# Kernel tuning notes

Hardware: AMD Instinct MI355X
Metric: run time of the kernel (lower is better)

Reference implementation:

```python
import jax, jax.numpy as jnp
import numpy as np

EPS = 1e-4

@jax.custom_vjp
def binarize(x):
    # BinaryConnectDeterministic: sign with sign(0)=+1
    return jnp.where(x >= 0, 1.0, -1.0).astype(x.dtype)

def _bin_fwd(x):
    return binarize(x), x

def _bin_bwd(x, g):
    # straight-through estimator, clipped to |x| <= 1
    return (g * (jnp.abs(x) <= 1).astype(g.dtype),)

binarize.defvjp(_bin_fwd, _bin_bwd)

def ap2(x):
    # approximate power-of-2: sign(x) * 2^round(log2|x|); grad is 0 a.e. (round/sign)
    a = jnp.maximum(jnp.abs(x), 1e-38)
    return jnp.sign(x) * jnp.exp2(jnp.round(jnp.log2(a)))

def shift_bn(x, gamma, beta, axes):
    # shift-based batch norm (BNN paper): var approximated via centered*AP2(centered),
    # inverse std and gamma replaced by their AP2 approximations. Training-mode batch stats.
    mean = jnp.mean(x, axis=axes, keepdims=True)
    c = x - mean
    var = jnp.mean(c * ap2(c), axis=axes, keepdims=True)
    xhat = c * ap2(1.0 / jnp.sqrt(var + EPS))
    shape = [1] * x.ndim
    shape[1] = x.shape[1]
    return ap2(gamma.reshape(shape)) * xhat + beta.reshape(shape)

def conv_bin(x, w, b):
    y = jax.lax.conv_general_dilated(x, binarize(w), (1, 1), [(1, 1), (1, 1)],
                                     dimension_numbers=('NCHW', 'OIHW', 'NCHW'))
    return y + b[None, :, None, None]

def maxpool3s2(x):
    return jax.lax.reduce_window(x, -jnp.inf, jax.lax.max,
                                 (1, 1, 3, 3), (1, 1, 2, 2), 'VALID')


def setup_inputs() -> dict:
    key = jax.random.key(0)
    ks = jax.random.split(key, 8)
    B, NU = 2048, 2048
    inp = {
        'x': jax.random.normal(ks[0], (B, 784), jnp.float32),
        'conv1_w': jax.random.normal(ks[1], (32, 1, 3, 3), jnp.float32) * 0.1,
        'conv1_b': jnp.zeros((32,), jnp.float32),
        'g1': jnp.ones((32,), jnp.float32), 'b1': jnp.zeros((32,), jnp.float32),
        'conv2_w': jax.random.normal(ks[2], (64, 32, 3, 3), jnp.float32) * 0.1,
        'conv2_b': jnp.zeros((64,), jnp.float32),
        'g2': jnp.ones((64,), jnp.float32), 'b2': jnp.zeros((64,), jnp.float32),
        'lin3_w': jax.random.normal(ks[3], (NU, 10816), jnp.float32) * 0.02,
        'lin3_b': jnp.zeros((NU,), jnp.float32),
        'g3': jnp.ones((NU,), jnp.float32), 'b3': jnp.zeros((NU,), jnp.float32),
        'lin4_w': jax.random.normal(ks[4], (10, NU), jnp.float32) * 0.02,
        'lin4_b': jnp.zeros((10,), jnp.float32),
    }
    return inp


def reference(x, conv1_w, conv1_b, g1, b1, conv2_w, conv2_b, g2, b2,
              lin3_w, lin3_b, g3, b3, lin4_w, lin4_b):
    h = x.reshape(-1, 1, 28, 28)
    h = jax.nn.relu(conv_bin(h, conv1_w, conv1_b))
    h = shift_bn(h, g1, b1, axes=(0, 2, 3))
    h = binarize(h)
    h = jax.nn.relu(conv_bin(h, conv2_w, conv2_b))
    h = maxpool3s2(h)                       # [B,64,13,13]
    h = shift_bn(h, g2, b2, axes=(0, 2, 3))
    h = binarize(h)
    h = h.reshape(h.shape[0], -1)           # [B,10816]
    h = jax.nn.relu(h @ binarize(lin3_w).T + lin3_b)
    h = shift_bn(h, g3, b3, axes=(0,))
    h = binarize(h)
    return h @ binarize(lin4_w).T + lin4_b  # [B,10] (no norm4/logsoftmax in forward)
```

## Files before the change

### kernel.cpp

```cpp
#include <hip/hip_runtime.h>

#define BB 2048
#define IMG 784
#define HWD 28
#define C1 32
#define C2 64
#define PP 169
#define PD 13
#define F3 10816
#define N3 2048
#define K4W 32
#define NOUT 10
#define CONV 27
#define PADW 30
#define OCCHUNK 8
#define IMGC 29
#define SCRP 740

typedef unsigned long long u64;
typedef int v4i __attribute__((ext_vector_type(4)));
typedef int v16i __attribute__((ext_vector_type(16)));

__device__ __forceinline__ float ap2mag(float c) {
    unsigned int a = __float_as_uint(c) & 0x7fffffffu;
    unsigned int e = (a >> 23) + ((a & 0x7fffffu) > 0x3504f3u);
    return __uint_as_float(e << 23);
}
__device__ __forceinline__ float ap2sgn(float g) {
    unsigned int u = __float_as_uint(g);
    unsigned int a = u & 0x7fffffffu;
    if (a == 0) return 0.f;
    unsigned int e = (a >> 23) + ((a & 0x7fffffu) > 0x3504f3u);
    return __uint_as_float((u & 0x80000000u) | (e << 23));
}

__global__ __launch_bounds__(256) void stage0(const float* __restrict__ x,
                                              const float* __restrict__ w1, const float* __restrict__ cb1,
                                              float* __restrict__ part1, float* __restrict__ w1b,
                                              const float* __restrict__ w2, char* __restrict__ w2i8,
                                              const float* __restrict__ w3, char* __restrict__ wp3i,
                                              const float* __restrict__ w4, u64* __restrict__ wp4) {
    __shared__ float xs[30 * PADW];
    __shared__ float red[4 * C1];
    int n = blockIdx.x, tid = threadIdx.x;
    int lane = tid & 63, wv = tid >> 6;
    {
        int idx = n * 256 + tid;
        int nthr = gridDim.x * 256;
        int total = (N3 * F3) / 4;
        for (int t = idx; t < total; t += nthr) {
            float4 wv4 = *(const float4*)(w3 + (size_t)t * 4);
            unsigned int w = (wv4.x >= 0.f ? 0x01u : 0xffu)
                           | (wv4.y >= 0.f ? 0x01u : 0xffu) << 8
                           | (wv4.z >= 0.f ? 0x01u : 0xffu) << 16
                           | (wv4.w >= 0.f ? 0x01u : 0xffu) << 24;
            *(unsigned int*)(wp3i + (size_t)t * 4) = w;
        }
    }
    if (n == 0) {
        for (int i = tid; i < C1 * 9; i += 256) w1b[i] = (w1[i] >= 0.f) ? 1.f : -1.f;
    } else if (n == 1) {
        for (int i = tid; i < 2 * 9 * 64 * 16; i += 256) {
            int hf = i / 9216;
            int r = i - hf * 9216;
            int t = r >> 10;
            int l = (r >> 4) & 63;
            int j = i & 15;
            int oc = hf * 32 + (l & 31);
            int ic = ((l >> 5) << 4) + j;
            w2i8[i] = (w2[oc * 288 + ic * 9 + t] >= 0.f) ? (char)1 : (char)(-1);
        }
    } else if (n == 2) {
        for (int w = wv; w < NOUT * K4W; w += 4) {
            int o = w / K4W, j = w % K4W;
            float wvl = w4[o * N3 + j * 64 + lane];
            u64 mask = __ballot(wvl >= 0.f);
            if (lane == 0) wp4[w] = mask;
        }
    }
    for (int i = tid; i < 30 * PADW; i += 256) {
        int r = i / PADW - 1, c = i % PADW - 1;
        float v = 0.f;
        if (r >= 0 && r < HWD && c >= 0 && c < HWD) v = x[n * IMG + r * HWD + c];
        xs[i] = v;
    }
    __syncthreads();
    bool act = tid < 196;
    int r = tid / 7, c0 = (tid % 7) * 4;
    float win[18];
#pragma unroll
    for (int k = 0; k < 18; k++) win[k] = 0.f;
    if (act) {
#pragma unroll
        for (int ry = 0; ry < 3; ry++)
#pragma unroll
            for (int cx = 0; cx < 6; cx++)
                win[ry * 6 + cx] = xs[(r + ry) * PADW + c0 + cx];
    }
#pragma unroll
    for (int ch = 0; ch < C1; ch++) {
        float a = 0.f;
        if (act) {
            float k0 = (w1[ch * 9 + 0] >= 0.f) ? 1.f : -1.f, k1 = (w1[ch * 9 + 1] >= 0.f) ? 1.f : -1.f;
            float k2 = (w1[ch * 9 + 2] >= 0.f) ? 1.f : -1.f, k3 = (w1[ch * 9 + 3] >= 0.f) ? 1.f : -1.f;
            float k4 = (w1[ch * 9 + 4] >= 0.f) ? 1.f : -1.f, k5 = (w1[ch * 9 + 5] >= 0.f) ? 1.f : -1.f;
            float k6 = (w1[ch * 9 + 6] >= 0.f) ? 1.f : -1.f, k7 = (w1[ch * 9 + 7] >= 0.f) ? 1.f : -1.f;
            float k8 = (w1[ch * 9 + 8] >= 0.f) ? 1.f : -1.f;
            float b = cb1[ch];
#pragma unroll
            for (int px = 0; px < 4; px++) {
                float s = win[px] * k0 + win[px + 1] * k1 + win[px + 2] * k2
                        + win[6 + px] * k3 + win[7 + px] * k4 + win[8 + px] * k5
                        + win[12 + px] * k6 + win[13 + px] * k7 + win[14 + px] * k8;
                a += fmaxf(s + b, 0.f);
            }
        }
        for (int off = 32; off; off >>= 1) a += __shfl_down(a, off);
        if (lane == 0) red[wv * C1 + ch] = a;
    }
    __syncthreads();
    if (tid < C1) part1[n * C1 + tid] = red[tid] + red[C1 + tid] + red[2 * C1 + tid] + red[3 * C1 + tid];
}

__global__ __launch_bounds__(256) void conv1_var(const float* __restrict__ x,
                            const float* __restrict__ w1b,
                            const float* __restrict__ cb1, const float* __restrict__ mean1,
                            float* __restrict__ part) {
    __shared__ float xs[30 * PADW];
    __shared__ float red[4 * C1];
    int n = blockIdx.x, tid = threadIdx.x;
    for (int i = tid; i < 30 * PADW; i += 256) {
        int r = i / PADW - 1, c = i % PADW - 1;
        float v = 0.f;
        if (r >= 0 && r < HWD && c >= 0 && c < HWD) v = x[n * IMG + r * HWD + c];
        xs[i] = v;
    }
    __syncthreads();
    bool act = tid < 196;
    int r = tid / 7, c0 = (tid % 7) * 4;
    float win[18];
#pragma unroll
    for (int k = 0; k < 18; k++) win[k] = 0.f;
    if (act) {
#pragma unroll
        for (int ry = 0; ry < 3; ry++)
#pragma unroll
            for (int cx = 0; cx < 6; cx++)
                win[ry * 6 + cx] = xs[(r + ry) * PADW + c0 + cx];
    }
    int lane = tid & 63, wv = tid >> 6;
#pragma unroll
    for (int ch = 0; ch < C1; ch++) {
        float a = 0.f;
        if (act) {
            float k0 = w1b[ch * 9 + 0], k1 = w1b[ch * 9 + 1], k2 = w1b[ch * 9 + 2];
            float k3 = w1b[ch * 9 + 3], k4 = w1b[ch * 9 + 4], k5 = w1b[ch * 9 + 5];
            float k6 = w1b[ch * 9 + 6], k7 = w1b[ch * 9 + 7], k8 = w1b[ch * 9 + 8];
            float b = cb1[ch], m = mean1[ch];
#pragma unroll
            for (int px = 0; px < 4; px++) {
                float s = win[px] * k0 + win[px + 1] * k1 + win[px + 2] * k2
                        + win[6 + px] * k3 + win[7 + px] * k4 + win[8 + px] * k5
                        + win[12 + px] * k6 + win[13 + px] * k7 + win[14 + px] * k8;
                float v = fmaxf(s + b, 0.f);
                float c = v - m;
                a += fabsf(c) * ap2mag(c);
            }
        }
        for (int off = 32; off; off >>= 1) a += __shfl_down(a, off);
        if (lane == 0) red[wv * C1 + ch] = a;
    }
    __syncthreads();
    if (tid < C1) part[n * C1 + tid] = red[tid] + red[C1 + tid] + red[2 * C1 + tid] + red[3 * C1 + tid];
}

__global__ __launch_bounds__(256) void conv1_pack(const float* __restrict__ x,
                           const float* __restrict__ w1b,
                           const float* __restrict__ cb1, const float* __restrict__ mean1,
                           const float* __restrict__ scale1, const float* __restrict__ beta1,
                           unsigned int* __restrict__ s1p) {
    __shared__ float xs[30 * PADW];
    int n = blockIdx.x, tid = threadIdx.x;
    for (int i = tid; i < 30 * PADW; i += 256) {
        int r = i / PADW - 1, c = i % PADW - 1;
        float v = 0.f;
        if (r >= 0 && r < HWD && c >= 0 && c < HWD) v = x[n * IMG + r * HWD + c];
        xs[i] = v;
    }
    __syncthreads();
    if (tid >= 196) return;
    int r = tid / 7, c0 = (tid % 7) * 4;
    float win[18];
#pragma unroll
    for (int ry = 0; ry < 3; ry++)
#pragma unroll
        for (int cx = 0; cx < 6; cx++)
            win[ry * 6 + cx] = xs[(r + ry) * PADW + c0 + cx];
    unsigned int bits0 = 0, bits1 = 0, bits2 = 0, bits3 = 0;
#pragma unroll
    for (int ch = 0; ch < C1; ch++) {
        float k0 = w1b[ch * 9 + 0], k1 = w1b[ch * 9 + 1], k2 = w1b[ch * 9 + 2];
        float k3 = w1b[ch * 9 + 3], k4 = w1b[ch * 9 + 4], k5 = w1b[ch * 9 + 5];
        float k6 = w1b[ch * 9 + 6], k7 = w1b[ch * 9 + 7], k8 = w1b[ch * 9 + 8];
        float b = cb1[ch], m = mean1[ch], sc = scale1[ch], bt = beta1[ch];
#pragma unroll
        for (int px = 0; px < 4; px++) {
            float s = win[px] * k0 + win[px + 1] * k1 + win[px + 2] * k2
                    + win[6 + px] * k3 + win[7 + px] * k4 + win[8 + px] * k5
                    + win[12 + px] * k6 + win[13 + px] * k7 + win[14 + px] * k8;
            float v = fmaxf(s + b, 0.f);
            float val = sc * (v - m) + bt;
            unsigned int bit = (val >= 0.f ? 1u : 0u) << ch;
            if (px == 0) bits0 |= bit;
            else if (px == 1) bits1 |= bit;
            else if (px == 2) bits2 |= bit;
            else bits3 |= bit;
        }
    }
    uint4 w4v = make_uint4(bits0, bits1, bits2, bits3);
    *reinterpret_cast<uint4*>(&s1p[n * IMG + r * HWD + c0]) = w4v;
}

__global__ __launch_bounds__(256) void conv2pool(const unsigned int* __restrict__ s1p,
                                                 const char* __restrict__ w2i8,
                                                 const float* __restrict__ cb2,
                                                 short* __restrict__ p2i,
                                                 float* __restrict__ part2) {
    __shared__ char img[IMGC * IMGC * 32];
    __shared__ short scr[32 * SCRP];
    __shared__ float psum[OCCHUNK * PP];
    __shared__ float pm[C2];
    int n = blockIdx.x, tid = threadIdx.x;
    int lane = tid & 63, wv = tid >> 6;
    for (int i = tid; i < IMGC * IMGC; i += 256) {
        int r = i / IMGC, c = i - r * IMGC;
        unsigned int w = 0u;
        if (r >= 1 && c >= 1) w = s1p[n * IMG + (r - 1) * HWD + (c - 1)];
        unsigned int d[8];
        if (r == 0 || c == 0) {
#pragma unroll
            for (int e = 0; e < 8; e++) d[e] = 0u;
        } else {
#pragma unroll
            for (int e = 0; e < 8; e++) {
                unsigned int nib = (w >> (4 * e)) & 0xFu;
                unsigned int t = (nib & 1u) | ((nib & 2u) << 7) | ((nib & 4u) << 14) | ((nib & 8u) << 21);
                d[e] = 0xFFFFFFFFu - t * 0xFEu;
            }
        }
        *(uint4*)&img[i * 32] = make_uint4(d[0], d[1], d[2], d[3]);
        *(uint4*)&img[i * 32 + 16] = make_uint4(d[4], d[5], d[6], d[7]);
    }
    __syncthreads();
    int hh = lane >> 5;
    int l31 = lane & 31;
    for (int hf = 0; hf < 2; hf++) {
        v4i bf[9];
#pragma unroll
        for (int t = 0; t < 9; t++)
            bf[t] = *(const v4i*)(w2i8 + (hf * 9 + t) * 1024 + lane * 16);
#pragma unroll
        for (int j = 0; j < 3; j++) {
            int mtA = wv + 8 * j, mtB = mtA + 4;
            int pA = mtA * 32 + l31; if (pA > 728) pA = 728;
            int pB = mtB * 32 + l31; if (pB > 728) pB = 728;
            int yA = pA / 27, xA = pA - yA * 27;
            int yB = pB / 27, xB = pB - yB * 27;
            int aA = (yA * IMGC + xA) * 32 + hh * 16;
            int aB = (yB * IMGC + xB) * 32 + hh * 16;
            v16i accA = {0,0,0,0,0,0,0,0,0,0,0,0,0,0,0,0};
            v16i accB = {0,0,0,0,0,0,0,0,0,0,0,0,0,0,0,0};
#pragma unroll
            for (int ky = 0; ky < 3; ky++)
#pragma unroll
                for (int kx = 0; kx < 3; kx++) {
                    v4i fA = *(const v4i*)&img[aA + (ky * IMGC + kx) * 32];
                    v4i fB = *(const v4i*)&img[aB + (ky * IMGC + kx) * 32];
                    accA = __builtin_amdgcn_mfma_i32_32x32x32_i8(fA, bf[ky * 3 + kx], accA, 0, 0, 0);
                    accB = __builtin_amdgcn_mfma_i32_32x32x32_i8(fB, bf[ky * 3 + kx], accB, 0, 0, 0);
                }
            short* sr = &scr[l31 * SCRP];
#pragma unroll
            for (int g = 0; g < 4; g++) {
                short4 sA;
                sA.x = (short)accA[4 * g + 0]; sA.y = (short)accA[4 * g + 1];
                sA.z = (short)accA[4 * g + 2]; sA.w = (short)accA[4 * g + 3];
                *(short4*)&sr[mtA * 32 + g * 8 + 4 * hh] = sA;
            }
            if (mtB < 23) {
#pragma unroll
                for (int g = 0; g < 4; g++) {
                    short4 sB;
                    sB.x = (short)accB[4 * g + 0]; sB.y = (short)accB[4 * g + 1];
                    sB.z = (short)accB[4 * g + 2]; sB.w = (short)accB[4 * g + 3];
                    *(short4*)&sr[mtB * 32 + g * 8 + 4 * hh] = sB;
                }
            }
        }
        __syncthreads();
        for (int base = 0; base < 32; base += OCCHUNK) {
            for (int q = tid; q < OCCHUNK * PP; q += 256) {
                int ol = q / PP, pix = q - ol * PP;
                int py = pix / PD, px = pix - py * PD;
                const short* rr = &scr[(base + ol) * SCRP + (2 * py) * CONV + 2 * px];
                int m0 = max(max((int)rr[0], (int)rr[1]), (int)rr[2]);
                int m1 = max(max((int)rr[CONV], (int)rr[CONV + 1]), (int)rr[CONV + 2]);
                int m2 = max(max((int)rr[2 * CONV], (int)rr[2 * CONV + 1]), (int)rr[2 * CONV + 2]);
                int val = max(max(m0, m1), m2);
                int oc = hf * 32 + base + ol;
                p2i[n * F3 + oc * PP + pix] = (short)val;
                psum[q] = fmaxf((float)val + cb2[oc], 0.f);
            }
            __syncthreads();
            for (int ol = wv; ol < OCCHUNK; ol += 4) {
                float a = 0.f;
                for (int pp = lane; pp < PP; pp += 64) a += psum[ol * PP + pp];
                for (int off = 32; off; off >>= 1) a += __shfl_down(a, off);
                if (lane == 0) pm[hf * 32 + base + ol] = a;
            }
            __syncthreads();
        }
    }
    if (tid < C2) part2[n * C2 + tid] = pm[tid];
}

__global__ __launch_bounds__(256) void p2_var(const short* __restrict__ p2i,
                         const float* __restrict__ cb2,
                         const float* __restrict__ mean2, float* __restrict__ part) {
    int n = blockIdx.x, tid = threadIdx.x, lane = tid & 63, wv = tid >> 6;
    const short* rowb = p2i + (size_t)n * F3;
    __shared__ float red[C2];
#pragma unroll
    for (int i = 0; i < 16; i++) {
        int ch = wv * 16 + i;
        const short* row = rowb + ch * PP;
        float b = cb2[ch];
        float m = mean2[ch];
        float a = 0.f;
        for (int p = lane; p < PP; p += 64) {
            float v = fmaxf((float)row[p] + b, 0.f);
            float c = v - m;
            a += fabsf(c) * ap2mag(c);
        }
        for (int off = 32; off; off >>= 1) a += __shfl_down(a, off);
        if (lane == 0) red[ch] = a;
    }
    __syncthreads();
    if (tid < C2) part[n * C2 + tid] = red[tid];
}

__global__ __launch_bounds__(256) void reduce_stats(const float* __restrict__ part, int nch, int nblk,
                             const float* __restrict__ g, float* __restrict__ outv,
                             int mode, double count) {
    int ch = blockIdx.x, tid = threadIdx.x;
    double a = 0.0;
    for (int i = tid; i < nblk; i += 256) a += (double)part[(size_t)i * nch + ch];
    __shared__ double red[4];
    for (int off = 32; off; off >>= 1) a += __shfl_down(a, off);
    int lane = tid & 63, wv = tid >> 6;
    if (lane == 0) red[wv] = a;
    __syncthreads();
    if (tid == 0) {
        double s = red[0] + red[1] + red[2] + red[3];
        if (mode == 0) {
            outv[ch] = (float)(s / count);
        } else {
            float var = (float)(s / count);
            float inv = 1.0f / sqrtf(var + 1e-4f);
            outv[ch] = ap2sgn(g[ch]) * ap2mag(inv);
        }
    }
}

__global__ __launch_bounds__(256) void p2_packi8(const short* __restrict__ p2i, const float* __restrict__ cb2,
                        const float* __restrict__ mean2, const float* __restrict__ scale2,
                        const float* __restrict__ beta2, char* __restrict__ hp3i) {
    int idx = blockIdx.x * 256 + threadIdx.x;
    int nthr = gridDim.x * 256;
    int total = (BB * F3) / 4;
    for (int t = idx; t < total; t += nthr) {
        int base = t * 4;
        int f0 = base % F3;
        unsigned int w = 0;
#pragma unroll
        for (int e = 0; e < 4; e++) {
            int f = f0 + e;
            int oc = f / PP;
            float v = fmaxf((float)p2i[base + e] + cb2[oc], 0.f);
            float val = scale2[oc] * (v - mean2[oc]) + beta2[oc];
            w |= (val >= 0.f ? 0x01u : 0xffu) << (8 * e);
        }
        *(unsigned int*)(hp3i + base) = w;
    }
}

__global__ __launch_bounds__(256) void lin3_mfma(const char* __restrict__ hp3i,
                                                 const char* __restrict__ wp3i,
                                                 const float* __restrict__ b3l,
                                                 float* __restrict__ h3,
                                                 float* __restrict__ part3) {
    __shared__ v4i aL[2][512];
    __shared__ v4i bL[2][256];
    __shared__ float csr[4][32];
    int tid = threadIdx.x;
    int lane = tid & 63, wv = tid >> 6;
    int wr = wv >> 1, wc = wv & 1;
    int m0 = blockIdx.y * 128, n0 = blockIdx.x * 64;
    int ra = tid >> 1, ha = tid & 1;
    const char* ag = hp3i + (size_t)(m0 + ra) * F3 + ha * 32;
    int abase = (ra >> 4) * 64 + (2 * ha) * 16 + (ra & 15);
    int rb = tid >> 2, qb = tid & 3;
    const char* bg = wp3i + (size_t)(n0 + rb) * F3 + qb * 16;
    int bbase = (rb >> 4) * 64 + qb * 16 + (rb & 15);
    v4i acc[4][2];
#pragma unroll
    for (int i = 0; i < 4; i++)
#pragma unroll
        for (int j = 0; j < 2; j++) acc[i][j] = (v4i){0, 0, 0, 0};
    v4i a0 = *(const v4i*)ag, a1 = *(const v4i*)(ag + 16);
    v4i b0 = *(const v4i*)bg;
    aL[0][abase] = a0; aL[0][abase + 16] = a1;
    bL[0][bbase] = b0;
    __syncthreads();
    for (int c = 0; c < 169; c++) {
        int cur = c & 1, nxt = cur ^ 1;
        if (c < 168) {
            ag += 64; bg += 64;
            a0 = *(const v4i*)ag; a1 = *(const v4i*)(ag + 16);
            b0 = *(const v4i*)bg;
        }
        v4i af[4], bf[2];
#pragma unroll
        for (int i = 0; i < 4; i++) af[i] = aL[cur][(wr * 4 + i) * 64 + lane];
#pragma unroll
        for (int j = 0; j < 2; j++) bf[j] = bL[cur][(wc * 2 + j) * 64 + lane];
#pragma unroll
        for (int i = 0; i < 4; i++)
#pragma unroll
            for (int j = 0; j < 2; j++)
                acc[i][j] = __builtin_amdgcn_mfma_i32_16x16x64_i8(af[i], bf[j], acc[i][j], 0, 0, 0);
        if (c < 168) {
            aL[nxt][abase] = a0; aL[nxt][abase + 16] = a1;
            bL[nxt][bbase] = b0;
        }
        __syncthreads();
    }
    int q = lane >> 4, m16 = lane & 15;
    float cs[2] = {0.f, 0.f};
#pragma unroll
    for (int j = 0; j < 2; j++) {
        int col = n0 + wc * 32 + j * 16 + m16;
        float bias = b3l[col];
#pragma unroll
        for (int i = 0; i < 4; i++) {
            int rowb = m0 + wr * 64 + i * 16 + q * 4;
#pragma unroll
            for (int rg = 0; rg < 4; rg++) {
                float v = fmaxf((float)acc[i][j][rg] + bias, 0.f);
                h3[(size_t)(rowb + rg) * N3 + col] = v;
                cs[j] += v;
            }
        }
    }
#pragma unroll
    for (int j = 0; j < 2; j++) {
        cs[j] += __shfl_xor(cs[j], 16);
        cs[j] += __shfl_xor(cs[j], 32);
        if (lane < 16) csr[wv][j * 16 + m16] = cs[j];
    }
    __syncthreads();
    if (tid < 64) {
        int wcc = tid >> 5, cc = tid & 31;
        part3[(size_t)blockIdx.y * N3 + n0 + tid] = csr[wcc][cc] + csr[2 + wcc][cc];
    }
}

__global__ __launch_bounds__(256) void h3_finish(const float* __restrict__ h3,
                                                 const float* __restrict__ part3,
                                                 const float* __restrict__ g3,
                                                 float* __restrict__ mean3, float* __restrict__ scale3) {
    int nn = blockIdx.x, tid = threadIdx.x;
    __shared__ float msh;
    __shared__ double redd[4];
    if (tid < 64) {
        float a = (tid < 16) ? part3[(size_t)tid * N3 + nn] : 0.f;
        for (int off = 8; off; off >>= 1) a += __shfl_down(a, off);
        if (tid == 0) { float m = a / (float)BB; mean3[nn] = m; msh = m; }
    }
    __syncthreads();
    float m = msh;
    float acc = 0.f;
#pragma unroll
    for (int q = 0; q < 8; q++) {
        float v = h3[(size_t)(q * 256 + tid) * N3 + nn];
        float c = v - m;
        acc += fabsf(c) * ap2mag(c);
    }
    double a = (double)acc;
    for (int off = 32; off; off >>= 1) a += __shfl_down(a, off);
    int lane = tid & 63, wv = tid >> 6;
    if (lane == 0) redd[wv] = a;
    __syncthreads();
    if (tid == 0) {
        float var = (float)((redd[0] + redd[1] + redd[2] + redd[3]) / (double)BB);
        float inv = 1.0f / sqrtf(var + 1e-4f);
        scale3[nn] = ap2sgn(g3[nn]) * ap2mag(inv);
    }
}

__global__ __launch_bounds__(256) void h4_out(const float* __restrict__ h3,
                                              const float* __restrict__ mean3, const float* __restrict__ scale3,
                                              const float* __restrict__ bt3,
                                              const u64* __restrict__ wp4, const float* __restrict__ b4,
                                              float* __restrict__ out) {
    __shared__ u64 hb[K4W];
    __shared__ u64 wsh[NOUT * 33];
    int m = blockIdx.x, tid = threadIdx.x, lane = tid & 63, wv = tid >> 6;
    for (int i = tid; i < NOUT * K4W; i += 256) wsh[(i / K4W) * 33 + (i % K4W)] = wp4[i];
#pragma unroll
    for (int q = 0; q < 8; q++) {
        int j = wv * 8 + q;
        int f = j * 64 + lane;
        float v = h3[(size_t)m * N3 + f];
        float val = scale3[f] * (v - mean3[f]) + bt3[f];
        u64 mask = __ballot(val >= 0.f);
        if (lane == 0) hb[j] = mask;
    }
    __syncthreads();
    if (tid < NOUT) {
        int c = 0;
#pragma unroll
        for (int k = 0; k < K4W; k++) c += (int)__popcll(hb[k] ^ wsh[tid * 33 + k]);
        out[m * NOUT + tid] = (float)(N3 - 2 * c) + b4[tid];
    }
}

extern "C" void kernel_launch(void* const* d_in, const int* in_sizes, int n_in,
                              void* d_out, int out_size, void* d_ws, size_t ws_size,
                              hipStream_t stream) {
    const float* x   = (const float*)d_in[0];
    const float* w1  = (const float*)d_in[1];
    const float* cb1 = (const float*)d_in[2];
    const float* g1  = (const float*)d_in[3];
    const float* bt1 = (const float*)d_in[4];
    const float* w2  = (const float*)d_in[5];
    const float* cb2 = (const float*)d_in[6];
    const float* g2  = (const float*)d_in[7];
    const float* bt2 = (const float*)d_in[8];
    const float* w3  = (const float*)d_in[9];
    const float* b3l = (const float*)d_in[10];
    const float* g3  = (const float*)d_in[11];
    const float* bt3 = (const float*)d_in[12];
    const float* w4  = (const float*)d_in[13];
    const float* b4l = (const float*)d_in[14];
    float* out = (float*)d_out;

    char* base = (char*)d_ws;
    size_t off = 0;
    auto carve = [&](size_t bytes) { char* p = base + off; off = (off + bytes + 255) & ~(size_t)255; return p; };
    char* bufA = carve((size_t)BB * C2 * PP * 2);
    char* bufB = carve((size_t)BB * F3);
    char* bufC = carve((size_t)N3 * F3);
    short* p2i         = (short*)bufA;
    float* h3          = (float*)bufA;
    char* hp3i         = bufB;
    unsigned int* s1p  = (unsigned int*)bufB;
    char* wp3i         = bufC;
    u64* wp4           = (u64*)carve((size_t)NOUT * K4W * 8);
    char* w2i8         = (char*)carve((size_t)2 * 9 * 64 * 16);
    float* w1b         = (float*)carve((size_t)C1 * 9 * 4);
    float* part1       = (float*)carve((size_t)BB * C1 * 4);
    float* part2       = (float*)carve((size_t)BB * C2 * 4);
    float* part3       = (float*)carve((size_t)16 * N3 * 4);
    float* fstats      = (float*)carve((size_t)(32 + 32 + 64 + 64 + 2048 + 2048) * 4);
    float* mean1 = fstats;          float* scale1 = fstats + 32;
    float* mean2 = fstats + 64;     float* scale2 = fstats + 128;
    float* mean3 = fstats + 192;    float* scale3 = fstats + 2240;

    stage0<<<BB, 256, 0, stream>>>(x, w1, cb1, part1, w1b, w2, w2i8, w3, wp3i, w4, wp4);
    reduce_stats<<<C1, 256, 0, stream>>>(part1, C1, BB, g1, mean1, 0, (double)BB * IMG);
    conv1_var<<<BB, 256, 0, stream>>>(x, w1b, cb1, mean1, part1);
    reduce_stats<<<C1, 256, 0, stream>>>(part1, C1, BB, g1, scale1, 1, (double)BB * IMG);
    conv1_pack<<<BB, 256, 0, stream>>>(x, w1b, cb1, mean1, scale1, bt1, s1p);
    conv2pool<<<BB, 256, 0, stream>>>(s1p, w2i8, cb2, p2i, part2);
    reduce_stats<<<C2, 256, 0, stream>>>(part2, C2, BB, g2, mean2, 0, (double)BB * PP);
    p2_var<<<BB, 256, 0, stream>>>(p2i, cb2, mean2, part2);
    reduce_stats<<<C2, 256, 0, stream>>>(part2, C2, BB, g2, scale2, 1, (double)BB * PP);
    p2_packi8<<<2048, 256, 0, stream>>>(p2i, cb2, mean2, scale2, bt2, hp3i);
    lin3_mfma<<<dim3(32, 16), 256, 0, stream>>>(hp3i, wp3i, b3l, h3, part3);
    h3_finish<<<N3, 256, 0, stream>>>(h3, part3, g3, mean3, scale3);
    h4_out<<<BB, 256, 0, stream>>>(h3, mean3, scale3, bt3, wp4, b4l, out);

    (void)in_sizes; (void)n_in; (void)out_size; (void)ws_size;
}
```

Measured before the change: 580.0 us.

## Use direct global-to-LDS loads in lin3 GEMM and write transposed h3 for stats

The int8 GEMM main loop now loads operand tiles with global_load_lds straight into shared memory, double-buffered over 128-byte K chunks, so tiles no longer pass through registers before the LDS store. This halves the number of barrier iterations and doubles the LDS footprint. The epilogue also writes a column-major copy of h3, so h3_finish can read each column contiguously instead of with a large stride. The cost is an extra 16 MB store and larger shared-memory use per block, which may reduce occupancy.

Result: faster. 549.9 us (-5.2%).

```diff
diff --git a/kernel.cpp b/kernel.cpp
--- a/kernel.cpp
+++ b/kernel.cpp
@@ -20,6 +20,10 @@
 typedef unsigned long long u64;
 typedef int v4i __attribute__((ext_vector_type(4)));
 typedef int v16i __attribute__((ext_vector_type(16)));
+
+#define GLOAD16(gp, lp) __builtin_amdgcn_global_load_lds( \
+    (__attribute__((address_space(1))) void*)(gp),        \
+    (__attribute__((address_space(3))) void*)(lp), 16, 0, 0)
 
 __device__ __forceinline__ float ap2mag(float c) {
     unsigned int a = __float_as_uint(c) & 0x7fffffffu;
@@ -398,50 +402,66 @@
                                                  const char* __restrict__ wp3i,
                                                  const float* __restrict__ b3l,
                                                  float* __restrict__ h3,
+                                                 float* __restrict__ h3T,
                                                  float* __restrict__ part3) {
-    __shared__ v4i aL[2][512];
-    __shared__ v4i bL[2][256];
+    __shared__ v4i aL[2][1024];
+    __shared__ v4i bL[2][512];
     __shared__ float csr[4][32];
     int tid = threadIdx.x;
     int lane = tid & 63, wv = tid >> 6;
     int wr = wv >> 1, wc = wv & 1;
     int m0 = blockIdx.y * 128, n0 = blockIdx.x * 64;
-    int ra = tid >> 1, ha = tid & 1;
-    const char* ag = hp3i + (size_t)(m0 + ra) * F3 + ha * 32;
-    int abase = (ra >> 4) * 64 + (2 * ha) * 16 + (ra & 15);
-    int rb = tid >> 2, qb = tid & 3;
-    const char* bg = wp3i + (size_t)(n0 + rb) * F3 + qb * 16;
-    int bbase = (rb >> 4) * 64 + qb * 16 + (rb & 15);
+    int loff = (lane & 15) * F3 + (lane >> 4) * 16;
+    const char* gA0 = hp3i + (size_t)(m0 + wv * 16) * F3 + loff;
+    const char* gA1 = gA0 + (size_t)64 * F3;
+    const char* gB0 = wp3i + (size_t)(n0 + wv * 16) * F3 + loff;
+    char* ldsA = (char*)&aL[0][0];
+    char* ldsB = (char*)&bL[0][0];
+    int sA = wv * 1024, sB = wv * 1024;
     v4i acc[4][2];
 #pragma unroll
     for (int i = 0; i < 4; i++)
 #pragma unroll
         for (int j = 0; j < 2; j++) acc[i][j] = (v4i){0, 0, 0, 0};
-    v4i a0 = *(const v4i*)ag, a1 = *(const v4i*)(ag + 16);
-    v4i b0 = *(const v4i*)bg;
-    aL[0][abase] = a0; aL[0][abase + 16] = a1;
-    bL[0][bbase] = b0;
-    __syncthreads();
-    for (int c = 0; c < 169; c++) {
-        int cur = c & 1, nxt = cur ^ 1;
-        if (c < 168) {
-            ag += 64; bg += 64;
-            a0 = *(const v4i*)ag; a1 = *(const v4i*)(ag + 16);
-            b0 = *(const v4i*)bg;
-        }
-        v4i af[4], bf[2];
-#pragma unroll
-        for (int i = 0; i < 4; i++) af[i] = aL[cur][(wr * 4 + i) * 64 + lane];
-#pragma unroll
-        for (int j = 0; j < 2; j++) bf[j] = bL[cur][(wc * 2 + j) * 64 + lane];
-#pragma unroll
-        for (int i = 0; i < 4; i++)
-#pragma unroll
-            for (int j = 0; j < 2; j++)
-                acc[i][j] = __builtin_amdgcn_mfma_i32_16x16x64_i8(af[i], bf[j], acc[i][j], 0, 0, 0);
-        if (c < 168) {
-            aL[nxt][abase] = a0; aL[nxt][abase + 16] = a1;
-            bL[nxt][bbase] = b0;
+    GLOAD16(gA0,      ldsA + sA);
+    GLOAD16(gA1,      ldsA + sA + 4096);
+    GLOAD16(gA0 + 64, ldsA + sA + 8192);
+    GLOAD16(gA1 + 64, ldsA + sA + 12288);
+    GLOAD16(gB0,      ldsB + sB);
+    GLOAD16(gB0 + 64, ldsB + sB + 4096);
+    __syncthreads();
+    for (int c = 0; c <= 84; ++c) {
+        int cur = c & 1;
+        if (c < 84) {
+            int nb = cur ^ 1;
+            const char* pA0 = gA0 + (size_t)(c + 1) * 128;
+            const char* pA1 = gA1 + (size_t)(c + 1) * 128;
+            const char* pB0 = gB0 + (size_t)(c + 1) * 128;
+            char* dA = ldsA + nb * 16384 + sA;
+            char* dB = ldsB + nb * 8192 + sB;
+            GLOAD16(pA0, dA);
+            GLOAD16(pA1, dA + 4096);
+            GLOAD16(pB0, dB);
+            if (c + 1 < 84) {
+                GLOAD16(pA0 + 64, dA + 8192);
+                GLOAD16(pA1 + 64, dA + 12288);
+                GLOAD16(pB0 + 64, dB + 4096);
+            }
+        }
+        const v4i* aC = &aL[cur][0];
+        const v4i* bC = &bL[cur][0];
+        int nks = (c == 84) ? 1 : 2;
+        for (int ks = 0; ks < nks; ++ks) {
+            v4i af[4], bf[2];
+#pragma unroll
+            for (int i = 0; i < 4; i++) af[i] = aC[ks * 512 + (wr * 4 + i) * 64 + lane];
+#pragma unroll
+            for (int j = 0; j < 2; j++) bf[j] = bC[ks * 256 + (wc * 2 + j) * 64 + lane];
+#pragma unroll
+            for (int i = 0; i < 4; i++)
+#pragma unroll
+                for (int j = 0; j < 2; j++)
+                    acc[i][j] = __builtin_amdgcn_mfma_i32_16x16x64_i8(af[i], bf[j], acc[i][j], 0, 0, 0);
         }
         __syncthreads();
     }
@@ -454,12 +474,15 @@
 #pragma unroll
         for (int i = 0; i < 4; i++) {
             int rowb = m0 + wr * 64 + i * 16 + q * 4;
+            float4 t4;
 #pragma unroll
             for (int rg = 0; rg < 4; rg++) {
                 float v = fmaxf((float)acc[i][j][rg] + bias, 0.f);
                 h3[(size_t)(rowb + rg) * N3 + col] = v;
+                ((float*)&t4)[rg] = v;
                 cs[j] += v;
             }
+            *(float4*)&h3T[(size_t)col * BB + rowb] = t4;
         }
     }
 #pragma unroll
@@ -475,7 +498,7 @@
     }
 }
 
-__global__ __launch_bounds__(256) void h3_finish(const float* __restrict__ h3,
+__global__ __launch_bounds__(256) void h3_finish(const float* __restrict__ h3T,
                                                  const float* __restrict__ part3,
                                                  const float* __restrict__ g3,
                                                  float* __restrict__ mean3, float* __restrict__ scale3) {
@@ -492,7 +515,7 @@
     float acc = 0.f;
 #pragma unroll
     for (int q = 0; q < 8; q++) {
-        float v = h3[(size_t)(q * 256 + tid) * N3 + nn];
+        float v = h3T[(size_t)nn * BB + q * 256 + tid];
         float c = v - m;
         acc += fabsf(c) * ap2mag(c);
     }
@@ -563,6 +586,7 @@
     char* bufC = carve((size_t)N3 * F3);
     short* p2i         = (short*)bufA;
     float* h3          = (float*)bufA;
+    float* h3T         = (float*)(bufA + (size_t)BB * N3 * 4);
     char* hp3i         = bufB;
     unsigned int* s1p  = (unsigned int*)bufB;
     char* wp3i         = bufC;
@@ -587,8 +611,8 @@
     p2_var<<<BB, 256, 0, stream>>>(p2i, cb2, mean2, part2);
     reduce_stats<<<C2, 256, 0, stream>>>(part2, C2, BB, g2, scale2, 1, (double)BB * PP);
     p2_packi8<<<2048, 256, 0, stream>>>(p2i, cb2, mean2, scale2, bt2, hp3i);
-    lin3_mfma<<<dim3(32, 16), 256, 0, stream>>>(hp3i, wp3i, b3l, h3, part3);
-    h3_finish<<<N3, 256, 0, stream>>>(h3, part3, g3, mean3, scale3);
+    lin3_mfma<<<dim3(32, 16), 256, 0, stream>>>(hp3i, wp3i, b3l, h3, h3T, part3);
+    h3_finish<<<N3, 256, 0, stream>>>(h3T, part3, g3, mean3, scale3);
     h4_out<<<BB, 256, 0, stream>>>(h3, mean3, scale3, bt3, wp4, b4l, out);
 
     (void)in_sizes; (void)n_in; (void)out_size; (void)ws_size;
```
